# Kernel optimization log

Measured on AMD Instinct MI355X. Metric: run time of the kernel, lower is better.

## Reference

```python
import jax, jax.numpy as jnp
import numpy as np
from jax import lax

B, N = 8, 8192
H, W = 512, 512
C = 192          # backbone feature channels (Swin-L stage 1)
HF, WF = 128, 128  # H/4, W/4
STATE = 256
VLR = 3
STRIDE = 4.0
DOWN = 4.0
EPS = 1e-8


def bilinear_sample(feat, poly, h, w):
    """F.grid_sample(align_corners=True, bilinear) equivalent.
    feat: (B,C,h,w), poly: (B,N,2) pixel coords -> (B,C,N)."""
    gx = poly[..., 0] / (w / 2.0) - 1.0
    gy = poly[..., 1] / (h / 2.0) - 1.0
    x = (gx + 1.0) * 0.5 * (w - 1)   # align_corners=True unnormalize
    y = (gy + 1.0) * 0.5 * (h - 1)
    x0 = jnp.floor(x); y0 = jnp.floor(y)
    fx = x - x0; fy = y - y0
    x0i = jnp.clip(x0, 0, w - 1).astype(jnp.int32)
    x1i = jnp.clip(x0 + 1, 0, w - 1).astype(jnp.int32)
    y0i = jnp.clip(y0, 0, h - 1).astype(jnp.int32)
    y1i = jnp.clip(y0 + 1, 0, h - 1).astype(jnp.int32)
    b = jnp.arange(feat.shape[0])[:, None]
    f00 = feat[b, :, y0i, x0i]  # (B,N,C)
    f01 = feat[b, :, y0i, x1i]
    f10 = feat[b, :, y1i, x0i]
    f11 = feat[b, :, y1i, x1i]
    w00 = ((1 - fy) * (1 - fx))[..., None]
    w01 = ((1 - fy) * fx)[..., None]
    w10 = (fy * (1 - fx))[..., None]
    w11 = (fy * fx)[..., None]
    out = f00 * w00 + f01 * w01 + f10 * w10 + f11 * w11  # (B,N,C)
    return jnp.transpose(out, (0, 2, 1))  # (B,C,N)


def mlp3(x, W1, b1, W2, b2, W3, b3):
    """per-point MLP (1x1 conv stack). x: (B,Cin,N) -> (B,Cout,N)."""
    h1 = jax.nn.relu(jnp.einsum('oc,bcn->bon', W1, x) + b1[None, :, None])
    h2 = jax.nn.relu(jnp.einsum('oc,bcn->bon', W2, h1) + b2[None, :, None])
    return jnp.einsum('oc,bcn->bon', W3, h2) + b3[None, :, None]


def can_poly(poly, mask):
    # canonical poly: subtract per-polygon masked min of valid points
    big = jnp.float32(1e9)
    masked = jnp.where(mask[..., None] > 0, poly, big)
    mins = jnp.min(masked, axis=1, keepdims=True)  # (B,1,2)
    return (poly - mins) * mask[..., None]


def polygon_angles(poly, mask):
    prev = jnp.roll(poly, 1, axis=1)
    nxt = jnp.roll(poly, -1, axis=1)
    v1 = prev - poly
    v2 = nxt - poly
    dot = jnp.sum(v1 * v2, axis=-1)
    nrm = jnp.linalg.norm(v1, axis=-1) * jnp.linalg.norm(v2, axis=-1)
    cosang = jnp.clip(dot / (nrm + EPS), -1.0, 1.0)
    return jnp.arccos(cosang) * mask  # (B,N)


def setup_inputs() -> dict:
    key = jax.random.key(0)
    ks = jax.random.split(key, 20)
    DIN_OFF = C + 2   # 194
    DIN_CLS = C + 3   # 195
    inp = {
        'image': jax.random.normal(ks[0], (B, 3, H, W), jnp.float32),
        'pred_points': jax.random.uniform(ks[1], (B, N, 2), jnp.float32) * (WF - 1),
        'valid_mask': jnp.ones((B, N), jnp.float32),
        'bw': jax.random.normal(ks[2], (C, 3, 4, 4), jnp.float32) * 0.05,
        'bb': jnp.zeros((C,), jnp.float32),
        'off_W1': jax.random.normal(ks[3], (VLR, STATE, DIN_OFF), jnp.float32) * 0.02,
        'off_b1': jnp.zeros((VLR, STATE), jnp.float32),
        'off_W2': jax.random.normal(ks[4], (VLR, STATE, STATE), jnp.float32) * 0.02,
        'off_b2': jnp.zeros((VLR, STATE), jnp.float32),
        'off_W3': jax.random.normal(ks[5], (VLR, 2, STATE), jnp.float32) * 0.02,
        'off_b3': jnp.zeros((VLR, 2), jnp.float32),
        'cls_W1': jax.random.normal(ks[6], (STATE, DIN_CLS), jnp.float32) * 0.02,
        'cls_b1': jnp.zeros((STATE,), jnp.float32),
        'cls_W2': jax.random.normal(ks[7], (STATE, STATE), jnp.float32) * 0.02,
        'cls_b2': jnp.zeros((STATE,), jnp.float32),
        'cls_W3': jax.random.normal(ks[8], (1, STATE), jnp.float32) * 0.02,
        'cls_b3': jnp.zeros((1,), jnp.float32),
    }
    return inp


def reference(image, pred_points, valid_mask, bw, bb,
              off_W1, off_b1, off_W2, off_b2, off_W3, off_b3,
              cls_W1, cls_b1, cls_W2, cls_b2, cls_W3, cls_b3):
    # frozen backbone stand-in (torch.no_grad on swin_l): stride-4 patch-embed conv
    feat = lax.conv_general_dilated(
        image, bw, window_strides=(4, 4), padding='VALID',
        dimension_numbers=('NCHW', 'OIHW', 'NCHW')) + bb[None, :, None, None]
    feat = lax.stop_gradient(feat)  # (B,C,HF,WF)

    py = pred_points
    for i in range(VLR):
        c_py = can_poly(py, valid_mask)
        g = bilinear_sample(feat, py, HF, WF) * valid_mask[:, None, :]   # (B,C,N)
        x = jnp.concatenate([g, jnp.transpose(c_py, (0, 2, 1))], axis=1)  # (B,C+2,N)
        off = mlp3(x, off_W1[i], off_b1[i], off_W2[i], off_b2[i], off_W3[i], off_b3[i])
        off = jnp.transpose(off, (0, 2, 1)) * valid_mask[..., None]      # (B,N,2)
        py = py + off * STRIDE

    gf = bilinear_sample(feat, py, HF, WF) * valid_mask[:, None, :]      # (B,C,N)
    angles = lax.stop_gradient(polygon_angles(py, valid_mask))           # (B,N)
    cls_feat = jnp.concatenate(
        [gf, jnp.transpose(py, (0, 2, 1)), angles[:, None, :]], axis=1)  # (B,C+3,N)
    logits = mlp3(cls_feat, cls_W1, cls_b1, cls_W2, cls_b2, cls_W3, cls_b3)  # (B,1,N)
    cls_points = logits[:, 0, :] * valid_mask                            # (B,N)

    final_refined_points = py * DOWN
    return (final_refined_points, cls_points)
```

## Files before the change

### kernel.cpp

```cpp
#include <hip/hip_runtime.h>
#include <hip/hip_bf16.h>
#include <hip/hip_fp8.h>

#define NB 8
#define NP 8192
#define IMH 512
#define IMW 512
#define NC 192
#define FH 128
#define FW 128
#define NSTATE 256

#define P1 232
#define P2 264
#define CPITCH 72
#define W1FRAG 57344
#define W2FRAG 65536

typedef __attribute__((ext_vector_type(8))) unsigned short ush8;
typedef __attribute__((ext_vector_type(8))) short short8v;
typedef __attribute__((ext_vector_type(4))) float f32x4;

__device__ __forceinline__ float fp8tof(unsigned char b) {
  __hip_fp8_e4m3 v;
  v.__x = b;
  return (float)v;
}
__device__ __forceinline__ unsigned char ftofp8(float f) {
  __hip_fp8_e4m3 v(f);
  return v.__x;
}
__device__ __forceinline__ unsigned fenc(float f) {
  unsigned u = __float_as_uint(f);
  return (u & 0x80000000u) ? ~u : (u | 0x80000000u);
}
__device__ __forceinline__ float fdec(unsigned u) {
  return __uint_as_float((u & 0x80000000u) ? (u & 0x7FFFFFFFu) : ~u);
}

__global__ __launch_bounds__(256) void conv_kernel(
    const float* __restrict__ img, const __hip_bfloat16* __restrict__ wcb,
    const float* __restrict__ bb, unsigned char* __restrict__ feat) {
  __shared__ __hip_bfloat16 Xim[64 * CPITCH];

  const int tid = threadIdx.x;
  const int lane = tid & 63;
  const int w = tid >> 6;
  const int cl = lane & 15;
  const int kg = lane >> 4;
  const int b = blockIdx.x & 7;
  const int pix0 = (blockIdx.x >> 3) * 64;
  const int y = pix0 >> 7;
  const int xh = (pix0 >> 6) & 1;

  {
    const int pix = tid & 63;
    const int q = tid >> 6;
    *(uint2*)&Xim[pix * CPITCH + 48 + q * 4] = (uint2){0u, 0u};
  }

#pragma unroll
  for (int it = 0; it < 3; ++it) {
    const int idx = it * 256 + tid;
    const int row = idx >> 6;
    const int c = idx & 63;
    const int ci = row >> 2, ky = row & 3;
    const float4 v = *(const float4*)(img + (((size_t)b * 3 + ci) * IMH +
                                             (y * 4 + ky)) * IMW + xh * 256 + c * 4);
    __hip_bfloat16 h[4];
    h[0] = __float2bfloat16(v.x);
    h[1] = __float2bfloat16(v.y);
    h[2] = __float2bfloat16(v.z);
    h[3] = __float2bfloat16(v.w);
    *(uint2*)&Xim[c * CPITCH + ci * 16 + ky * 4] = *(const uint2*)h;
  }
  __syncthreads();

  f32x4 acc[4][3];
#pragma unroll
  for (int mt = 0; mt < 4; ++mt)
#pragma unroll
    for (int nt = 0; nt < 3; ++nt) acc[mt][nt] = (f32x4){0, 0, 0, 0};

#pragma unroll
  for (int kc = 0; kc < 2; ++kc) {
    short8v af[4], bfv[3];
#pragma unroll
    for (int mt = 0; mt < 4; ++mt)
      af[mt] = *(const short8v*)&Xim[(mt * 16 + cl) * CPITCH + kc * 32 + kg * 8];
#pragma unroll
    for (int nt = 0; nt < 3; ++nt)
      bfv[nt] = *(const short8v*)&wcb[(size_t)(w * 48 + nt * 16 + cl) * 64 +
                                      kc * 32 + kg * 8];
#pragma unroll
    for (int mt = 0; mt < 4; ++mt)
#pragma unroll
      for (int nt = 0; nt < 3; ++nt)
        acc[mt][nt] = __builtin_amdgcn_mfma_f32_16x16x32_bf16(
            af[mt], bfv[nt], acc[mt][nt], 0, 0, 0);
  }

#pragma unroll
  for (int nt = 0; nt < 3; ++nt) {
    const float bias = bb[w * 48 + nt * 16 + cl];
#pragma unroll
    for (int mt = 0; mt < 4; ++mt) {
#pragma unroll
      for (int r = 0; r < 4; ++r) {
        feat[((size_t)b * 16384 + pix0 + mt * 16 + kg * 4 + r) * 192 +
             w * 48 + nt * 16 + cl] = ftofp8(acc[mt][nt][r] + bias);
      }
    }
  }
}

__global__ void prep_all_kernel(
    const float* __restrict__ oW1, const float* __restrict__ cW1,
    const float* __restrict__ oW2, const float* __restrict__ cW2,
    const float* __restrict__ bw, const float* __restrict__ pred,
    const float* __restrict__ mask, __hip_bfloat16* __restrict__ w1c,
    __hip_bfloat16* __restrict__ w2c, __hip_bfloat16* __restrict__ wcb,
    unsigned* __restrict__ mins4) {
  __shared__ float sx[4], sy[4];
  const int idx = blockIdx.x * 256 + threadIdx.x;
  const int region = blockIdx.y;
  if (region == 0) {
    if (idx >= 4 * W1FRAG) return;
    const int L = idx / W1FRAG;
    const int rem = idx - L * W1FRAG;
    const int kc = rem >> 13;
    const int r2 = rem & 8191;
    const int ng = r2 >> 9;
    const int r3 = r2 & 511;
    const int lane = r3 >> 3;
    const int e = r3 & 7;
    const int n = ng * 16 + (lane & 15);
    const int k = kc * 32 + (lane >> 4) * 8 + e;
    const float* src = (L < 3) ? (oW1 + (size_t)L * 256 * 194) : cW1;
    const int K = (L < 3) ? 194 : 195;
    w1c[idx] = __float2bfloat16((k < K) ? src[(size_t)n * K + k] : 0.0f);
  } else if (region == 1) {
    if (idx >= 4 * W2FRAG) return;
    const int L = idx >> 16;
    const int rem = idx & 65535;
    const int kc = rem >> 13;
    const int r2 = rem & 8191;
    const int ng = r2 >> 9;
    const int r3 = r2 & 511;
    const int lane = r3 >> 3;
    const int e = r3 & 7;
    const int n = ng * 16 + (lane & 15);
    const int k = kc * 32 + (lane >> 4) * 8 + e;
    const float* src = (L < 3) ? (oW2 + (size_t)L * 65536) : cW2;
    w2c[idx] = __float2bfloat16(src[(size_t)n * 256 + k]);
  } else if (region == 2) {
    if (idx < 48) mins4[16 + idx] = fenc(1e9f);
    if (idx >= 192 * 64) return;
    const int n = idx >> 6;
    const int k = idx & 63;
    wcb[idx] = __float2bfloat16((k < 48) ? bw[(size_t)n * 48 + k] : 0.0f);
  } else {
    if (blockIdx.x >= 8) return;
    const int b = blockIdx.x;
    float mx = 1e9f, my = 1e9f;
    for (int n = threadIdx.x; n < NP; n += 256) {
      float m = mask[(size_t)b * NP + n];
      float2 p = *(const float2*)&pred[((size_t)b * NP + n) * 2];
      mx = fminf(mx, m > 0.0f ? p.x : 1e9f);
      my = fminf(my, m > 0.0f ? p.y : 1e9f);
    }
#pragma unroll
    for (int o = 32; o > 0; o >>= 1) {
      mx = fminf(mx, __shfl_down(mx, o));
      my = fminf(my, __shfl_down(my, o));
    }
    if ((threadIdx.x & 63) == 0) {
      sx[threadIdx.x >> 6] = mx;
      sy[threadIdx.x >> 6] = my;
    }
    __syncthreads();
    if (threadIdx.x == 0) {
      mx = fminf(fminf(sx[0], sx[1]), fminf(sx[2], sx[3]));
      my = fminf(fminf(sy[0], sy[1]), fminf(sy[2], sy[3]));
      mins4[b * 2 + 0] = fenc(mx);
      mins4[b * 2 + 1] = fenc(my);
    }
  }
}

template <bool CLS>
__global__ __launch_bounds__(256) void mlp_kernel(
    const unsigned char* __restrict__ feat,
    const float* __restrict__ p_in,
    const float* __restrict__ mask,
    const unsigned* __restrict__ mins_in,
    unsigned* __restrict__ mins_out,
    const __hip_bfloat16* __restrict__ W1c, const float* __restrict__ b1,
    const __hip_bfloat16* __restrict__ W2c, const float* __restrict__ b2,
    const float* __restrict__ W3, const float* __restrict__ b3,
    float* __restrict__ out0) {
  __shared__ __hip_bfloat16 Xls[64 * P2];
  __shared__ float red[4][64][2];

  const int tid = threadIdx.x;
  const int lane = tid & 63;
  const int w = tid >> 6;
  const int cl = lane & 15;
  const int kg = lane >> 4;
  const int b = blockIdx.x & 7;
  const int m0 = (blockIdx.x >> 3) * 64;

  {
    const int m = tid >> 2;
    const int s = tid & 3;
    const int n = m0 + m;
    const size_t pidx = (size_t)b * NP + n;
    const float msk = mask[pidx];
    const float2 pv = *(const float2*)&p_in[pidx * 2];
    const float px = pv.x, pyv = pv.y;
    const float xs = px * (127.0f / 128.0f);
    const float ys = pyv * (127.0f / 128.0f);
    const float x0f = floorf(xs), y0f = floorf(ys);
    const float fx = xs - x0f, fy = ys - y0f;
    const int x0 = (int)fminf(fmaxf(x0f, 0.0f), 127.0f);
    const int x1 = (int)fminf(fmaxf(x0f + 1.0f, 0.0f), 127.0f);
    const int y0 = (int)fminf(fmaxf(y0f, 0.0f), 127.0f);
    const int y1 = (int)fminf(fmaxf(y0f + 1.0f, 0.0f), 127.0f);
    const float w00 = (1.0f - fy) * (1.0f - fx);
    const float w01 = (1.0f - fy) * fx;
    const float w10 = fy * (1.0f - fx);
    const float w11 = fy * fx;
    const unsigned char* fb = feat + (size_t)b * 16384 * 192 + s * 16;
    const unsigned char* r00 = fb + (size_t)(y0 * FW + x0) * 192;
    const unsigned char* r01 = fb + (size_t)(y0 * FW + x1) * 192;
    const unsigned char* r10 = fb + (size_t)(y1 * FW + x0) * 192;
    const unsigned char* r11 = fb + (size_t)(y1 * FW + x1) * 192;
#pragma unroll
    for (int v = 0; v < 3; ++v) {
      union { uint4 u; unsigned char c[16]; } a0, a1, a2, a3;
      a0.u = *(const uint4*)(r00 + v * 64);
      a1.u = *(const uint4*)(r01 + v * 64);
      a2.u = *(const uint4*)(r10 + v * 64);
      a3.u = *(const uint4*)(r11 + v * 64);
      __hip_bfloat16 h[16];
#pragma unroll
      for (int e = 0; e < 16; ++e) {
        float gg = w00 * fp8tof(a0.c[e]) + w01 * fp8tof(a1.c[e]) +
                   w10 * fp8tof(a2.c[e]) + w11 * fp8tof(a3.c[e]);
        h[e] = __float2bfloat16(gg * msk);
      }
      *(ush8*)&Xls[m * P1 + v * 64 + s * 16 + 0] = *(const ush8*)&h[0];
      *(ush8*)&Xls[m * P1 + v * 64 + s * 16 + 8] = *(const ush8*)&h[8];
    }
    if (s == 0) {
      __hip_bfloat16 ex[32];
#pragma unroll
      for (int i = 0; i < 32; ++i) ex[i] = __float2bfloat16(0.0f);
      if constexpr (!CLS) {
        ex[0] = __float2bfloat16((px - fdec(mins_in[b * 2 + 0])) * msk);
        ex[1] = __float2bfloat16((pyv - fdec(mins_in[b * 2 + 1])) * msk);
      } else {
        ex[0] = __float2bfloat16(px);
        ex[1] = __float2bfloat16(pyv);
        const int npv = (n + NP - 1) & (NP - 1);
        const int nnx = (n + 1) & (NP - 1);
        const float2 pp = *(const float2*)&p_in[((size_t)b * NP + npv) * 2];
        const float2 pn = *(const float2*)&p_in[((size_t)b * NP + nnx) * 2];
        const float v1x = pp.x - px, v1y = pp.y - pyv;
        const float v2x = pn.x - px, v2y = pn.y - pyv;
        const float dot = v1x * v2x + v1y * v2y;
        const float nrm =
            sqrtf(v1x * v1x + v1y * v1y) * sqrtf(v2x * v2x + v2y * v2y);
        const float ca = fminf(fmaxf(dot / (nrm + 1e-8f), -1.0f), 1.0f);
        ex[2] = __float2bfloat16(acosf(ca) * msk);
      }
#pragma unroll
      for (int q = 0; q < 4; ++q)
        *(ush8*)&Xls[m * P1 + 192 + q * 8] = *(const ush8*)&ex[q * 8];
    }
  }

  float b1v[4], b2v[4], w3av[4], w3bv[4];
#pragma unroll
  for (int nt = 0; nt < 4; ++nt) {
    const int n = w * 64 + nt * 16 + cl;
    b1v[nt] = b1[n];
    b2v[nt] = b2[n];
    w3av[nt] = W3[n];
    w3bv[nt] = CLS ? 0.0f : W3[256 + n];
  }
  __syncthreads();

  f32x4 acc[4][4];
#pragma unroll
  for (int mt = 0; mt < 4; ++mt)
#pragma unroll
    for (int nt = 0; nt < 4; ++nt) acc[mt][nt] = (f32x4){0, 0, 0, 0};

#pragma unroll
  for (int kc = 0; kc < 7; ++kc) {
    short8v af[4], bfv[4];
#pragma unroll
    for (int nt = 0; nt < 4; ++nt)
      bfv[nt] = *(const short8v*)&W1c[kc * 8192 + (w * 4 + nt) * 512 + lane * 8];
#pragma unroll
    for (int mt = 0; mt < 4; ++mt)
      af[mt] = *(const short8v*)&Xls[(mt * 16 + cl) * P1 + kc * 32 + kg * 8];
#pragma unroll
    for (int mt = 0; mt < 4; ++mt)
#pragma unroll
      for (int nt = 0; nt < 4; ++nt)
        acc[mt][nt] = __builtin_amdgcn_mfma_f32_16x16x32_bf16(
            af[mt], bfv[nt], acc[mt][nt], 0, 0, 0);
  }
  __syncthreads();

#pragma unroll
  for (int nt = 0; nt < 4; ++nt) {
    const float bias = b1v[nt];
    const int n = w * 64 + nt * 16 + cl;
#pragma unroll
    for (int mt = 0; mt < 4; ++mt) {
#pragma unroll
      for (int r = 0; r < 4; ++r) {
        const float v = fmaxf(acc[mt][nt][r] + bias, 0.0f);
        Xls[(mt * 16 + kg * 4 + r) * P2 + n] = __float2bfloat16(v);
      }
    }
  }
  __syncthreads();

  f32x4 acc2[4][4];
#pragma unroll
  for (int mt = 0; mt < 4; ++mt)
#pragma unroll
    for (int nt = 0; nt < 4; ++nt) acc2[mt][nt] = (f32x4){0, 0, 0, 0};

#pragma unroll
  for (int kc = 0; kc < 8; ++kc) {
    short8v af[4], bfv[4];
#pragma unroll
    for (int nt = 0; nt < 4; ++nt)
      bfv[nt] = *(const short8v*)&W2c[kc * 8192 + (w * 4 + nt) * 512 + lane * 8];
#pragma unroll
    for (int mt = 0; mt < 4; ++mt)
      af[mt] = *(const short8v*)&Xls[(mt * 16 + cl) * P2 + kc * 32 + kg * 8];
#pragma unroll
    for (int mt = 0; mt < 4; ++mt)
#pragma unroll
      for (int nt = 0; nt < 4; ++nt)
        acc2[mt][nt] = __builtin_amdgcn_mfma_f32_16x16x32_bf16(
            af[mt], bfv[nt], acc2[mt][nt], 0, 0, 0);
  }

  float pr[4][4][2];
#pragma unroll
  for (int mt = 0; mt < 4; ++mt)
#pragma unroll
    for (int r = 0; r < 4; ++r) { pr[mt][r][0] = 0.0f; pr[mt][r][1] = 0.0f; }

#pragma unroll
  for (int nt = 0; nt < 4; ++nt) {
    const float bias = b2v[nt];
    const float w3a = w3av[nt];
    const float w3b = w3bv[nt];
#pragma unroll
    for (int mt = 0; mt < 4; ++mt) {
#pragma unroll
      for (int r = 0; r < 4; ++r) {
        const float t = fmaxf(acc2[mt][nt][r] + bias, 0.0f);
        pr[mt][r][0] = fmaf(t, w3a, pr[mt][r][0]);
        if constexpr (!CLS) pr[mt][r][1] = fmaf(t, w3b, pr[mt][r][1]);
      }
    }
  }
#pragma unroll
  for (int s = 1; s < 16; s <<= 1) {
#pragma unroll
    for (int mt = 0; mt < 4; ++mt)
#pragma unroll
      for (int r = 0; r < 4; ++r) {
        pr[mt][r][0] += __shfl_xor(pr[mt][r][0], s);
        if constexpr (!CLS) pr[mt][r][1] += __shfl_xor(pr[mt][r][1], s);
      }
  }
  if constexpr (!CLS) {
    if (cl < 8) {
      const int r = cl >> 1, o = cl & 1;
#pragma unroll
      for (int mt = 0; mt < 4; ++mt)
        red[w][mt * 16 + kg * 4 + r][o] = pr[mt][r][o];
    }
  } else {
    if (cl < 4) {
      const int r = cl;
#pragma unroll
      for (int mt = 0; mt < 4; ++mt)
        red[w][mt * 16 + kg * 4 + r][0] = pr[mt][r][0];
    }
  }
  __syncthreads();

  if constexpr (!CLS) {
    if (tid < 128) {
      const int m = tid >> 1, o = tid & 1;
      const float s = red[0][m][o] + red[1][m][o] + red[2][m][o] + red[3][m][o];
      const size_t pidx = (size_t)b * NP + m0 + m;
      const float msk = mask[pidx];
      const float off = (s + b3[o]) * msk;
      const float nv = p_in[pidx * 2 + o] + off * 4.0f;
      out0[pidx * 2 + o] = nv;
      float mval = (msk > 0.0f) ? nv : 1e9f;
#pragma unroll
      for (int st = 2; st < 64; st <<= 1)
        mval = fminf(mval, __shfl_xor(mval, st));
      if ((tid & 63) < 2 && mins_out != nullptr)
        atomicMin(&mins_out[b * 2 + o], fenc(mval));
    }
  } else {
    if (tid < 64) {
      const int m = tid;
      const float s = red[0][m][0] + red[1][m][0] + red[2][m][0] + red[3][m][0];
      const size_t pidx = (size_t)b * NP + m0 + m;
      const float msk = mask[pidx];
      out0[pidx * 2 + 0] = p_in[pidx * 2 + 0] * 4.0f;
      out0[pidx * 2 + 1] = p_in[pidx * 2 + 1] * 4.0f;
      out0[(size_t)2 * NB * NP + pidx] = (s + b3[0]) * msk;
    }
  }
}

extern "C" void kernel_launch(void* const* d_in, const int* in_sizes, int n_in,
                              void* d_out, int out_size, void* d_ws,
                              size_t ws_size, hipStream_t stream) {
  const float* image = (const float*)d_in[0];
  const float* pred  = (const float*)d_in[1];
  const float* mask  = (const float*)d_in[2];
  const float* bw    = (const float*)d_in[3];
  const float* bb    = (const float*)d_in[4];
  const float* oW1   = (const float*)d_in[5];
  const float* ob1   = (const float*)d_in[6];
  const float* oW2   = (const float*)d_in[7];
  const float* ob2   = (const float*)d_in[8];
  const float* oW3   = (const float*)d_in[9];
  const float* ob3   = (const float*)d_in[10];
  const float* cW1   = (const float*)d_in[11];
  const float* cb1   = (const float*)d_in[12];
  const float* cW2   = (const float*)d_in[13];
  const float* cb2   = (const float*)d_in[14];
  const float* cW3   = (const float*)d_in[15];
  const float* cb3   = (const float*)d_in[16];
  float* out = (float*)d_out;

  char* ws = (char*)d_ws;
  unsigned char* feat = (unsigned char*)ws;
  const size_t featB = (size_t)NB * FH * FW * NC;
  float* pyA  = (float*)(ws + featB);
  float* pyB  = pyA + (size_t)NB * NP * 2;
  unsigned* mins4 = (unsigned*)(pyB + (size_t)NB * NP * 2);
  __hip_bfloat16* w1c = (__hip_bfloat16*)(mins4 + 64);
  __hip_bfloat16* w2c = w1c + (size_t)4 * W1FRAG;
  __hip_bfloat16* wcb = w2c + (size_t)4 * W2FRAG;

  prep_all_kernel<<<dim3(1024, 4), 256, 0, stream>>>(
      oW1, cW1, oW2, cW2, bw, pred, mask, w1c, w2c, wcb, mins4);
  conv_kernel<<<dim3(NB * 16384 / 64), 256, 0, stream>>>(image, wcb, bb, feat);

  const float* cur = pred;
  float* nxt = pyA;
  for (int i = 0; i < 3; ++i) {
    mlp_kernel<false><<<dim3(NB * NP / 64), 256, 0, stream>>>(
        feat, cur, mask, mins4 + i * 16,
        (i < 2) ? (mins4 + (i + 1) * 16) : nullptr,
        w1c + (size_t)i * W1FRAG, ob1 + (size_t)i * NSTATE,
        w2c + (size_t)i * W2FRAG, ob2 + (size_t)i * NSTATE,
        oW3 + (size_t)i * 2 * NSTATE, ob3 + (size_t)i * 2, nxt);
    cur = nxt;
    nxt = (nxt == pyA) ? pyB : pyA;
  }
  mlp_kernel<true><<<dim3(NB * NP / 64), 256, 0, stream>>>(
      feat, cur, mask, nullptr, nullptr, w1c + (size_t)3 * W1FRAG, cb1,
      w2c + (size_t)3 * W2FRAG, cb2, cW3, cb3, out);
}
```

Before: 190.8 us.

## Process two point tiles per block, prefetching second gather during first GEMM

Each MLP block now handles 128 points as two 64-point tiles with double-buffered shared memory. The fp8 feature gather for the second tile is issued before the first tile's GEMMs, so global latency can overlap MFMA work, and the grid is halved. The costs are doubled LDS per block (about 67KB), more live registers for the prefetched payload, and lower occupancy and parallelism, since only 512 blocks are launched.

Result: slower. 221.6 us (+16.2%).

```diff
diff --git a/kernel.cpp b/kernel.cpp
--- a/kernel.cpp
+++ b/kernel.cpp
@@ -188,6 +188,11 @@
   }
 }
 
+struct GC {
+  const unsigned char *r00, *r01, *r10, *r11;
+  float w00, w01, w10, w11, msk, px, py;
+};
+
 template <bool CLS>
 __global__ __launch_bounds__(256) void mlp_kernel(
     const unsigned char* __restrict__ feat,
@@ -199,7 +204,7 @@
     const __hip_bfloat16* __restrict__ W2c, const float* __restrict__ b2,
     const float* __restrict__ W3, const float* __restrict__ b3,
     float* __restrict__ out0) {
-  __shared__ __hip_bfloat16 Xls[64 * P2];
+  __shared__ __hip_bfloat16 Xls[2][64 * P2];
   __shared__ float red[4][64][2];
 
   const int tid = threadIdx.x;
@@ -208,77 +213,92 @@
   const int cl = lane & 15;
   const int kg = lane >> 4;
   const int b = blockIdx.x & 7;
-  const int m0 = (blockIdx.x >> 3) * 64;
-
-  {
-    const int m = tid >> 2;
-    const int s = tid & 3;
-    const int n = m0 + m;
+  const int m0 = (blockIdx.x >> 3) * 128;
+  const int m = tid >> 2;
+  const int s = tid & 3;
+
+  auto mkgc = [&](int n) {
+    GC g;
     const size_t pidx = (size_t)b * NP + n;
-    const float msk = mask[pidx];
+    g.msk = mask[pidx];
     const float2 pv = *(const float2*)&p_in[pidx * 2];
-    const float px = pv.x, pyv = pv.y;
-    const float xs = px * (127.0f / 128.0f);
-    const float ys = pyv * (127.0f / 128.0f);
+    g.px = pv.x;
+    g.py = pv.y;
+    const float xs = g.px * (127.0f / 128.0f);
+    const float ys = g.py * (127.0f / 128.0f);
     const float x0f = floorf(xs), y0f = floorf(ys);
     const float fx = xs - x0f, fy = ys - y0f;
     const int x0 = (int)fminf(fmaxf(x0f, 0.0f), 127.0f);
     const int x1 = (int)fminf(fmaxf(x0f + 1.0f, 0.0f), 127.0f);
     const int y0 = (int)fminf(fmaxf(y0f, 0.0f), 127.0f);
     const int y1 = (int)fminf(fmaxf(y0f + 1.0f, 0.0f), 127.0f);
-    const float w00 = (1.0f - fy) * (1.0f - fx);
-    const float w01 = (1.0f - fy) * fx;
-    const float w10 = fy * (1.0f - fx);
-    const float w11 = fy * fx;
+    g.w00 = (1.0f - fy) * (1.0f - fx);
+    g.w01 = (1.0f - fy) * fx;
+    g.w10 = fy * (1.0f - fx);
+    g.w11 = fy * fx;
     const unsigned char* fb = feat + (size_t)b * 16384 * 192 + s * 16;
-    const unsigned char* r00 = fb + (size_t)(y0 * FW + x0) * 192;
-    const unsigned char* r01 = fb + (size_t)(y0 * FW + x1) * 192;
-    const unsigned char* r10 = fb + (size_t)(y1 * FW + x0) * 192;
-    const unsigned char* r11 = fb + (size_t)(y1 * FW + x1) * 192;
+    g.r00 = fb + (size_t)(y0 * FW + x0) * 192;
+    g.r01 = fb + (size_t)(y0 * FW + x1) * 192;
+    g.r10 = fb + (size_t)(y1 * FW + x0) * 192;
+    g.r11 = fb + (size_t)(y1 * FW + x1) * 192;
+    return g;
+  };
+
+  auto ldpay = [&](const GC& g, uint4* p0, uint4* p1, uint4* p2, uint4* p3) {
+#pragma unroll
+    for (int v = 0; v < 3; ++v) {
+      p0[v] = *(const uint4*)(g.r00 + v * 64);
+      p1[v] = *(const uint4*)(g.r01 + v * 64);
+      p2[v] = *(const uint4*)(g.r10 + v * 64);
+      p3[v] = *(const uint4*)(g.r11 + v * 64);
+    }
+  };
+
+  auto cvstore = [&](const GC& g, const uint4* p0, const uint4* p1,
+                     const uint4* p2, const uint4* p3, __hip_bfloat16* X) {
 #pragma unroll
     for (int v = 0; v < 3; ++v) {
       union { uint4 u; unsigned char c[16]; } a0, a1, a2, a3;
-      a0.u = *(const uint4*)(r00 + v * 64);
-      a1.u = *(const uint4*)(r01 + v * 64);
-      a2.u = *(const uint4*)(r10 + v * 64);
-      a3.u = *(const uint4*)(r11 + v * 64);
+      a0.u = p0[v]; a1.u = p1[v]; a2.u = p2[v]; a3.u = p3[v];
       __hip_bfloat16 h[16];
 #pragma unroll
       for (int e = 0; e < 16; ++e) {
-        float gg = w00 * fp8tof(a0.c[e]) + w01 * fp8tof(a1.c[e]) +
-                   w10 * fp8tof(a2.c[e]) + w11 * fp8tof(a3.c[e]);
-        h[e] = __float2bfloat16(gg * msk);
-      }
-      *(ush8*)&Xls[m * P1 + v * 64 + s * 16 + 0] = *(const ush8*)&h[0];
-      *(ush8*)&Xls[m * P1 + v * 64 + s * 16 + 8] = *(const ush8*)&h[8];
-    }
-    if (s == 0) {
-      __hip_bfloat16 ex[32];
-#pragma unroll
-      for (int i = 0; i < 32; ++i) ex[i] = __float2bfloat16(0.0f);
-      if constexpr (!CLS) {
-        ex[0] = __float2bfloat16((px - fdec(mins_in[b * 2 + 0])) * msk);
-        ex[1] = __float2bfloat16((pyv - fdec(mins_in[b * 2 + 1])) * msk);
-      } else {
-        ex[0] = __float2bfloat16(px);
-        ex[1] = __float2bfloat16(pyv);
-        const int npv = (n + NP - 1) & (NP - 1);
-        const int nnx = (n + 1) & (NP - 1);
-        const float2 pp = *(const float2*)&p_in[((size_t)b * NP + npv) * 2];
-        const float2 pn = *(const float2*)&p_in[((size_t)b * NP + nnx) * 2];
-        const float v1x = pp.x - px, v1y = pp.y - pyv;
-        const float v2x = pn.x - px, v2y = pn.y - pyv;
-        const float dot = v1x * v2x + v1y * v2y;
-        const float nrm =
-            sqrtf(v1x * v1x + v1y * v1y) * sqrtf(v2x * v2x + v2y * v2y);
-        const float ca = fminf(fmaxf(dot / (nrm + 1e-8f), -1.0f), 1.0f);
-        ex[2] = __float2bfloat16(acosf(ca) * msk);
-      }
-#pragma unroll
-      for (int q = 0; q < 4; ++q)
-        *(ush8*)&Xls[m * P1 + 192 + q * 8] = *(const ush8*)&ex[q * 8];
-    }
-  }
+        float gg = g.w00 * fp8tof(a0.c[e]) + g.w01 * fp8tof(a1.c[e]) +
+                   g.w10 * fp8tof(a2.c[e]) + g.w11 * fp8tof(a3.c[e]);
+        h[e] = __float2bfloat16(gg * g.msk);
+      }
+      *(ush8*)&X[m * P1 + v * 64 + s * 16 + 0] = *(const ush8*)&h[0];
+      *(ush8*)&X[m * P1 + v * 64 + s * 16 + 8] = *(const ush8*)&h[8];
+    }
+  };
+
+  auto extras = [&](const GC& g, int n, __hip_bfloat16* X) {
+    if (s != 0) return;
+    __hip_bfloat16 ex[32];
+#pragma unroll
+    for (int i = 0; i < 32; ++i) ex[i] = __float2bfloat16(0.0f);
+    if constexpr (!CLS) {
+      ex[0] = __float2bfloat16((g.px - fdec(mins_in[b * 2 + 0])) * g.msk);
+      ex[1] = __float2bfloat16((g.py - fdec(mins_in[b * 2 + 1])) * g.msk);
+    } else {
+      ex[0] = __float2bfloat16(g.px);
+      ex[1] = __float2bfloat16(g.py);
+      const int npv = (n + NP - 1) & (NP - 1);
+      const int nnx = (n + 1) & (NP - 1);
+      const float2 pp = *(const float2*)&p_in[((size_t)b * NP + npv) * 2];
+      const float2 pn = *(const float2*)&p_in[((size_t)b * NP + nnx) * 2];
+      const float v1x = pp.x - g.px, v1y = pp.y - g.py;
+      const float v2x = pn.x - g.px, v2y = pn.y - g.py;
+      const float dot = v1x * v2x + v1y * v2y;
+      const float nrm =
+          sqrtf(v1x * v1x + v1y * v1y) * sqrtf(v2x * v2x + v2y * v2y);
+      const float ca = fminf(fmaxf(dot / (nrm + 1e-8f), -1.0f), 1.0f);
+      ex[2] = __float2bfloat16(acosf(ca) * g.msk);
+    }
+#pragma unroll
+    for (int q = 0; q < 4; ++q)
+      *(ush8*)&X[m * P1 + 192 + q * 8] = *(const ush8*)&ex[q * 8];
+  };
 
   float b1v[4], b2v[4], w3av[4], w3bv[4];
 #pragma unroll
@@ -289,145 +309,171 @@
     w3av[nt] = W3[n];
     w3bv[nt] = CLS ? 0.0f : W3[256 + n];
   }
+
+  auto gemms = [&](__hip_bfloat16* X, int tm0) {
+    f32x4 acc[4][4];
+#pragma unroll
+    for (int mt = 0; mt < 4; ++mt)
+#pragma unroll
+      for (int nt = 0; nt < 4; ++nt) acc[mt][nt] = (f32x4){0, 0, 0, 0};
+
+#pragma unroll
+    for (int kc = 0; kc < 7; ++kc) {
+      short8v af[4], bfv[4];
+#pragma unroll
+      for (int nt = 0; nt < 4; ++nt)
+        bfv[nt] =
+            *(const short8v*)&W1c[kc * 8192 + (w * 4 + nt) * 512 + lane * 8];
+#pragma unroll
+      for (int mt = 0; mt < 4; ++mt)
+        af[mt] = *(const short8v*)&X[(mt * 16 + cl) * P1 + kc * 32 + kg * 8];
+#pragma unroll
+      for (int mt = 0; mt < 4; ++mt)
+#pragma unroll
+        for (int nt = 0; nt < 4; ++nt)
+          acc[mt][nt] = __builtin_amdgcn_mfma_f32_16x16x32_bf16(
+              af[mt], bfv[nt], acc[mt][nt], 0, 0, 0);
+    }
+    __syncthreads();
+
+#pragma unroll
+    for (int nt = 0; nt < 4; ++nt) {
+      const float bias = b1v[nt];
+      const int n = w * 64 + nt * 16 + cl;
+#pragma unroll
+      for (int mt = 0; mt < 4; ++mt) {
+#pragma unroll
+        for (int r = 0; r < 4; ++r) {
+          const float v = fmaxf(acc[mt][nt][r] + bias, 0.0f);
+          X[(mt * 16 + kg * 4 + r) * P2 + n] = __float2bfloat16(v);
+        }
+      }
+    }
+    __syncthreads();
+
+    f32x4 acc2[4][4];
+#pragma unroll
+    for (int mt = 0; mt < 4; ++mt)
+#pragma unroll
+      for (int nt = 0; nt < 4; ++nt) acc2[mt][nt] = (f32x4){0, 0, 0, 0};
+
+#pragma unroll
+    for (int kc = 0; kc < 8; ++kc) {
+      short8v af[4], bfv[4];
+#pragma unroll
+      for (int nt = 0; nt < 4; ++nt)
+        bfv[nt] =
+            *(const short8v*)&W2c[kc * 8192 + (w * 4 + nt) * 512 + lane * 8];
+#pragma unroll
+      for (int mt = 0; mt < 4; ++mt)
+        af[mt] = *(const short8v*)&X[(mt * 16 + cl) * P2 + kc * 32 + kg * 8];
+#pragma unroll
+      for (int mt = 0; mt < 4; ++mt)
+#pragma unroll
+        for (int nt = 0; nt < 4; ++nt)
+          acc2[mt][nt] = __builtin_amdgcn_mfma_f32_16x16x32_bf16(
+              af[mt], bfv[nt], acc2[mt][nt], 0, 0, 0);
+    }
+
+    float pr[4][4][2];
+#pragma unroll
+    for (int mt = 0; mt < 4; ++mt)
+#pragma unroll
+      for (int r = 0; r < 4; ++r) { pr[mt][r][0] = 0.0f; pr[mt][r][1] = 0.0f; }
+
+#pragma unroll
+    for (int nt = 0; nt < 4; ++nt) {
+      const float bias = b2v[nt];
+      const float w3a = w3av[nt];
+      const float w3b = w3bv[nt];
+#pragma unroll
+      for (int mt = 0; mt < 4; ++mt) {
+#pragma unroll
+        for (int r = 0; r < 4; ++r) {
+          const float t = fmaxf(acc2[mt][nt][r] + bias, 0.0f);
+          pr[mt][r][0] = fmaf(t, w3a, pr[mt][r][0]);
+          if constexpr (!CLS) pr[mt][r][1] = fmaf(t, w3b, pr[mt][r][1]);
+        }
+      }
+    }
+#pragma unroll
+    for (int st = 1; st < 16; st <<= 1) {
+#pragma unroll
+      for (int mt = 0; mt < 4; ++mt)
+#pragma unroll
+        for (int r = 0; r < 4; ++r) {
+          pr[mt][r][0] += __shfl_xor(pr[mt][r][0], st);
+          if constexpr (!CLS) pr[mt][r][1] += __shfl_xor(pr[mt][r][1], st);
+        }
+    }
+    if constexpr (!CLS) {
+      if (cl < 8) {
+        const int r = cl >> 1, o = cl & 1;
+#pragma unroll
+        for (int mt = 0; mt < 4; ++mt)
+          red[w][mt * 16 + kg * 4 + r][o] = pr[mt][r][o];
+      }
+    } else {
+      if (cl < 4) {
+        const int r = cl;
+#pragma unroll
+        for (int mt = 0; mt < 4; ++mt)
+          red[w][mt * 16 + kg * 4 + r][0] = pr[mt][r][0];
+      }
+    }
+    __syncthreads();
+
+    if constexpr (!CLS) {
+      if (tid < 128) {
+        const int mm = tid >> 1, o = tid & 1;
+        const float sv =
+            red[0][mm][o] + red[1][mm][o] + red[2][mm][o] + red[3][mm][o];
+        const size_t pidx = (size_t)b * NP + tm0 + mm;
+        const float msk = mask[pidx];
+        const float off = (sv + b3[o]) * msk;
+        const float nv = p_in[pidx * 2 + o] + off * 4.0f;
+        out0[pidx * 2 + o] = nv;
+        float mval = (msk > 0.0f) ? nv : 1e9f;
+#pragma unroll
+        for (int st = 2; st < 64; st <<= 1)
+          mval = fminf(mval, __shfl_xor(mval, st));
+        if ((tid & 63) < 2 && mins_out != nullptr)
+          atomicMin(&mins_out[b * 2 + o], fenc(mval));
+      }
+    } else {
+      if (tid < 64) {
+        const int mm = tid;
+        const float sv =
+            red[0][mm][0] + red[1][mm][0] + red[2][mm][0] + red[3][mm][0];
+        const size_t pidx = (size_t)b * NP + tm0 + mm;
+        const float msk = mask[pidx];
+        out0[pidx * 2 + 0] = p_in[pidx * 2 + 0] * 4.0f;
+        out0[pidx * 2 + 1] = p_in[pidx * 2 + 1] * 4.0f;
+        out0[(size_t)2 * NB * NP + pidx] = (sv + b3[0]) * msk;
+      }
+    }
+  };
+
+  uint4 pa0[3], pa1[3], pa2[3], pa3[3];
+  {
+    GC ga = mkgc(m0 + m);
+    ldpay(ga, pa0, pa1, pa2, pa3);
+    cvstore(ga, pa0, pa1, pa2, pa3, Xls[0]);
+    extras(ga, m0 + m, Xls[0]);
+  }
   __syncthreads();
 
-  f32x4 acc[4][4];
-#pragma unroll
-  for (int mt = 0; mt < 4; ++mt)
-#pragma unroll
-    for (int nt = 0; nt < 4; ++nt) acc[mt][nt] = (f32x4){0, 0, 0, 0};
-
-#pragma unroll
-  for (int kc = 0; kc < 7; ++kc) {
-    short8v af[4], bfv[4];
-#pragma unroll
-    for (int nt = 0; nt < 4; ++nt)
-      bfv[nt] = *(const short8v*)&W1c[kc * 8192 + (w * 4 + nt) * 512 + lane * 8];
-#pragma unroll
-    for (int mt = 0; mt < 4; ++mt)
-      af[mt] = *(const short8v*)&Xls[(mt * 16 + cl) * P1 + kc * 32 + kg * 8];
-#pragma unroll
-    for (int mt = 0; mt < 4; ++mt)
-#pragma unroll
-      for (int nt = 0; nt < 4; ++nt)
-        acc[mt][nt] = __builtin_amdgcn_mfma_f32_16x16x32_bf16(
-            af[mt], bfv[nt], acc[mt][nt], 0, 0, 0);
-  }
+  uint4 pb0[3], pb1[3], pb2[3], pb3[3];
+  GC gb = mkgc(m0 + 64 + m);
+  ldpay(gb, pb0, pb1, pb2, pb3);
+
+  gemms(Xls[0], m0);
+
+  cvstore(gb, pb0, pb1, pb2, pb3, Xls[1]);
+  extras(gb, m0 + 64 + m, Xls[1]);
   __syncthreads();
 
-#pragma unroll
-  for (int nt = 0; nt < 4; ++nt) {
-    const float bias = b1v[nt];
-    const int n = w * 64 + nt * 16 + cl;
-#pragma unroll
-    for (int mt = 0; mt < 4; ++mt) {
-#pragma unroll
-      for (int r = 0; r < 4; ++r) {
-        const float v = fmaxf(acc[mt][nt][r] + bias, 0.0f);
-        Xls[(mt * 16 + kg * 4 + r) * P2 + n] = __float2bfloat16(v);
-      }
-    }
-  }
-  __syncthreads();
-
-  f32x4 acc2[4][4];
-#pragma unroll
-  for (int mt = 0; mt < 4; ++mt)
-#pragma unroll
-    for (int nt = 0; nt < 4; ++nt) acc2[mt][nt] = (f32x4){0, 0, 0, 0};
-
-#pragma unroll
-  for (int kc = 0; kc < 8; ++kc) {
-    short8v af[4], bfv[4];
-#pragma unroll
-    for (int nt = 0; nt < 4; ++nt)
-      bfv[nt] = *(const short8v*)&W2c[kc * 8192 + (w * 4 + nt) * 512 + lane * 8];
-#pragma unroll
-    for (int mt = 0; mt < 4; ++mt)
-      af[mt] = *(const short8v*)&Xls[(mt * 16 + cl) * P2 + kc * 32 + kg * 8];
-#pragma unroll
-    for (int mt = 0; mt < 4; ++mt)
-#pragma unroll
-      for (int nt = 0; nt < 4; ++nt)
-        acc2[mt][nt] = __builtin_amdgcn_mfma_f32_16x16x32_bf16(
-            af[mt], bfv[nt], acc2[mt][nt], 0, 0, 0);
-  }
-
-  float pr[4][4][2];
-#pragma unroll
-  for (int mt = 0; mt < 4; ++mt)
-#pragma unroll
-    for (int r = 0; r < 4; ++r) { pr[mt][r][0] = 0.0f; pr[mt][r][1] = 0.0f; }
-
-#pragma unroll
-  for (int nt = 0; nt < 4; ++nt) {
-    const float bias = b2v[nt];
-    const float w3a = w3av[nt];
-    const float w3b = w3bv[nt];
-#pragma unroll
-    for (int mt = 0; mt < 4; ++mt) {
-#pragma unroll
-      for (int r = 0; r < 4; ++r) {
-        const float t = fmaxf(acc2[mt][nt][r] + bias, 0.0f);
-        pr[mt][r][0] = fmaf(t, w3a, pr[mt][r][0]);
-        if constexpr (!CLS) pr[mt][r][1] = fmaf(t, w3b, pr[mt][r][1]);
-      }
-    }
-  }
-#pragma unroll
-  for (int s = 1; s < 16; s <<= 1) {
-#pragma unroll
-    for (int mt = 0; mt < 4; ++mt)
-#pragma unroll
-      for (int r = 0; r < 4; ++r) {
-        pr[mt][r][0] += __shfl_xor(pr[mt][r][0], s);
-        if constexpr (!CLS) pr[mt][r][1] += __shfl_xor(pr[mt][r][1], s);
-      }
-  }
-  if constexpr (!CLS) {
-    if (cl < 8) {
-      const int r = cl >> 1, o = cl & 1;
-#pragma unroll
-      for (int mt = 0; mt < 4; ++mt)
-        red[w][mt * 16 + kg * 4 + r][o] = pr[mt][r][o];
-    }
-  } else {
-    if (cl < 4) {
-      const int r = cl;
-#pragma unroll
-      for (int mt = 0; mt < 4; ++mt)
-        red[w][mt * 16 + kg * 4 + r][0] = pr[mt][r][0];
-    }
-  }
-  __syncthreads();
-
-  if constexpr (!CLS) {
-    if (tid < 128) {
-      const int m = tid >> 1, o = tid & 1;
-      const float s = red[0][m][o] + red[1][m][o] + red[2][m][o] + red[3][m][o];
-      const size_t pidx = (size_t)b * NP + m0 + m;
-      const float msk = mask[pidx];
-      const float off = (s + b3[o]) * msk;
-      const float nv = p_in[pidx * 2 + o] + off * 4.0f;
-      out0[pidx * 2 + o] = nv;
-      float mval = (msk > 0.0f) ? nv : 1e9f;
-#pragma unroll
-      for (int st = 2; st < 64; st <<= 1)
-        mval = fminf(mval, __shfl_xor(mval, st));
-      if ((tid & 63) < 2 && mins_out != nullptr)
-        atomicMin(&mins_out[b * 2 + o], fenc(mval));
-    }
-  } else {
-    if (tid < 64) {
-      const int m = tid;
-      const float s = red[0][m][0] + red[1][m][0] + red[2][m][0] + red[3][m][0];
-      const size_t pidx = (size_t)b * NP + m0 + m;
-      const float msk = mask[pidx];
-      out0[pidx * 2 + 0] = p_in[pidx * 2 + 0] * 4.0f;
-      out0[pidx * 2 + 1] = p_in[pidx * 2 + 1] * 4.0f;
-      out0[(size_t)2 * NB * NP + pidx] = (s + b3[0]) * msk;
-    }
-  }
+  gemms(Xls[1], m0 + 64);
 }
 
 extern "C" void kernel_launch(void* const* d_in, const int* in_sizes, int n_in,
@@ -469,7 +515,7 @@
   const float* cur = pred;
   float* nxt = pyA;
   for (int i = 0; i < 3; ++i) {
-    mlp_kernel<false><<<dim3(NB * NP / 64), 256, 0, stream>>>(
+    mlp_kernel<false><<<dim3(NB * NP / 128), 256, 0, stream>>>(
         feat, cur, mask, mins4 + i * 16,
         (i < 2) ? (mins4 + (i + 1) * 16) : nullptr,
         w1c + (size_t)i * W1FRAG, ob1 + (size_t)i * NSTATE,
@@ -478,7 +524,7 @@
     cur = nxt;
     nxt = (nxt == pyA) ? pyB : pyA;
   }
-  mlp_kernel<true><<<dim3(NB * NP / 64), 256, 0, stream>>>(
+  mlp_kernel<true><<<dim3(NB * NP / 128), 256, 0, stream>>>(
       feat, cur, mask, nullptr, nullptr, w1c + (size_t)3 * W1FRAG, cb1,
       w2c + (size_t)3 * W2FRAG, cb2, cW3, cb3, out);
 }
```
